# Performance work log

Hardware: AMD Instinct MI355X
Metric: run time of the kernel (lower is better)

The kernel has to match this reference:

```python
import jax, jax.numpy as jnp
import numpy as np

N_NODES = 50000
BN_EPS = 1e-5


def setup_inputs() -> dict:
    key = jax.random.key(0)
    ks = jax.random.split(key, 16)
    N, IN, H, OUT, E = N_NODES, 512, 128, 64, 800000
    s = lambda fi, fo: 1.0 / np.sqrt(fi)
    inp = {
        'x': jax.random.normal(ks[0], (N, IN), dtype=jnp.float32),
        'edge_index': jax.random.randint(ks[1], (2, E), 0, N, dtype=jnp.int32),
        # mlpA: Linear(N -> H)
        'WA': jax.random.uniform(ks[2], (H, N), jnp.float32, -s(N, H), s(N, H)),
        'bA': jax.random.uniform(ks[3], (H,), jnp.float32, -s(N, H), s(N, H)),
        # mlpX: Linear(IN -> H)
        'WX': jax.random.uniform(ks[4], (H, IN), jnp.float32, -s(IN, H), s(IN, H)),
        'bX': jax.random.uniform(ks[5], (H,), jnp.float32, -s(IN, H), s(IN, H)),
        # W: Linear(2H -> H)
        'W': jax.random.uniform(ks[6], (H, 2 * H), jnp.float32, -s(2 * H, H), s(2 * H, H)),
        'bW': jax.random.uniform(ks[7], (H,), jnp.float32, -s(2 * H, H), s(2 * H, H)),
        # mlp_final layer 1: Linear(H -> H) + BN
        'Wf1': jax.random.uniform(ks[8], (H, H), jnp.float32, -s(H, H), s(H, H)),
        'bf1': jax.random.uniform(ks[9], (H,), jnp.float32, -s(H, H), s(H, H)),
        'gamma': jnp.ones((H,), jnp.float32),
        'beta': jnp.zeros((H,), jnp.float32),
        # mlp_final layer 2: Linear(H -> OUT)
        'Wf2': jax.random.uniform(ks[10], (OUT, H), jnp.float32, -s(H, OUT), s(H, OUT)),
        'bf2': jax.random.uniform(ks[11], (OUT,), jnp.float32, -s(H, OUT), s(H, OUT)),
    }
    return inp


def _batchnorm(x, gamma, beta):
    # training-mode BN over the node/batch axis (biased variance, as in torch)
    mean = jnp.mean(x, axis=0)
    var = jnp.var(x, axis=0)
    return (x - mean) * jax.lax.rsqrt(var + BN_EPS) * gamma + beta


def reference(x, edge_index, WA, bA, WX, bX, W, bW, Wf1, bf1, gamma, beta, Wf2, bf2):
    row, col = edge_index[0], edge_index[1]
    row = row - row.min()
    # xA = A @ WA.T + bA  where A[i,j]=1 per (row,col) edge (duplicates sum).
    # Equivalent SpMM: gather columns of WA at `col`, segment-sum into `row`.
    xA = jax.ops.segment_sum(WA.T[col], row, num_segments=N_NODES) + bA  # [N, H]
    xX = x @ WX.T + bX  # [N, H]
    h = jnp.concatenate([xA, xX], axis=-1) @ W.T + bW  # [N, H]
    h = jax.nn.relu(h + xA + xX)
    # mlp_final (num_layers=2): Linear -> ReLU -> BN -> (dropout off) -> Linear
    h = jax.nn.relu(h @ Wf1.T + bf1)
    h = _batchnorm(h, gamma, beta)
    out = h @ Wf2.T + bf2  # [N, OUT]
    return out
```

## Files before the change

### kernel.cpp

```cpp
#include <hip/hip_runtime.h>

typedef __bf16 bf16_t;
typedef __bf16 bf16x8 __attribute__((ext_vector_type(8)));
typedef float f32x4 __attribute__((ext_vector_type(4)));

#define IN_DIM 512
#define H_DIM 128
#define OUT_DIM 64
#define BN_EPS 1e-5f
#define SCAN_BLK 2048

__device__ __forceinline__ float ld_adapt(const void* p, size_t i, int isbf) {
    return isbf ? (float)((const bf16_t*)p)[i] : ((const float*)p)[i];
}

__device__ __forceinline__ void split8(const float* __restrict__ p, bf16x8& hi, bf16x8& lo) {
    f32x4 v0 = *(const f32x4*)p;
    f32x4 v1 = *(const f32x4*)(p + 4);
#pragma unroll
    for (int i = 0; i < 8; ++i) {
        float f = (i < 4) ? v0[i] : v1[i - 4];
        bf16_t h = (bf16_t)f;
        hi[i] = h;
        lo[i] = (bf16_t)(f - (float)h);
    }
}

__global__ void k_init(const void* bA, const void* bX, const void* bW, const void* bf1,
                       const void* gamma, const void* beta, const void* bf2,
                       float* __restrict__ dst, int* __restrict__ flag) {
    __shared__ int s_isbf;
    if (threadIdx.x == 0) {
        unsigned u = *(const unsigned*)gamma;
        int f = (u == 0x3F803F80u) ? 1 : 0;
        *flag = f;
        s_isbf = f;
    }
    __syncthreads();
    int isbf = s_isbf;
    int t = threadIdx.x;
    dst[t] = ld_adapt(bA, t, isbf);
    dst[128 + t] = ld_adapt(bX, t, isbf);
    dst[256 + t] = ld_adapt(bW, t, isbf);
    dst[384 + t] = ld_adapt(bf1, t, isbf);
    dst[512 + t] = ld_adapt(gamma, t, isbf);
    dst[640 + t] = ld_adapt(beta, t, isbf);
    if (t < OUT_DIM) dst[768 + t] = ld_adapt(bf2, t, isbf);
}

__global__ __launch_bounds__(256) void k_transpose(const void* __restrict__ WA,
                                                   float* __restrict__ WAT, int N,
                                                   const int* __restrict__ flag) {
    __shared__ float t[64][130];
    int isbf = *flag;
    int n0 = blockIdx.x * 64;
    int tid = threadIdx.x;
#pragma unroll
    for (int i = 0; i < 32; ++i) {
        int lin = i * 256 + tid;
        int h = lin >> 6, nl = lin & 63;
        int n = n0 + nl;
        t[nl][h] = (n < N) ? ld_adapt(WA, (size_t)h * N + n, isbf) : 0.f;
    }
    __syncthreads();
#pragma unroll
    for (int i = 0; i < 32; ++i) {
        int lin = i * 256 + tid;
        int nl = lin >> 7, h = lin & 127;
        int n = n0 + nl;
        if (n < N) WAT[(size_t)n * H_DIM + h] = t[nl][h];
    }
}

__global__ __launch_bounds__(256) void k_prep(const int* __restrict__ rows, int E,
                                              int* __restrict__ bmin, int* __restrict__ cnt) {
    __shared__ int sm[4];
    int i = blockIdx.x * 256 + threadIdx.x;
    int m = 0x7fffffff;
    if (i < E) {
        int r = rows[i];
        m = r;
        atomicAdd(&cnt[r], 1);
    }
    for (int off = 32; off; off >>= 1) m = min(m, __shfl_xor(m, off, 64));
    if ((threadIdx.x & 63) == 0) sm[threadIdx.x >> 6] = m;
    __syncthreads();
    if (threadIdx.x == 0)
        bmin[blockIdx.x] = min(min(sm[0], sm[1]), min(sm[2], sm[3]));
}

__global__ __launch_bounds__(256) void k_scan1(const int* __restrict__ cnt,
                                               int* __restrict__ offs,
                                               int* __restrict__ bsum, int N) {
    __shared__ int ts[256];
    int base = blockIdx.x * SCAN_BLK;
    int t = threadIdx.x;
    int v[8], s = 0;
#pragma unroll
    for (int i = 0; i < 8; ++i) {
        int idx = base + t * 8 + i;
        v[i] = (idx < N) ? cnt[idx] : 0;
        s += v[i];
    }
    ts[t] = s;
    __syncthreads();
    for (int off = 1; off < 256; off <<= 1) {
        int x = (t >= off) ? ts[t - off] : 0;
        __syncthreads();
        ts[t] += x;
        __syncthreads();
    }
    int run = ts[t] - s;
#pragma unroll
    for (int i = 0; i < 8; ++i) {
        int idx = base + t * 8 + i;
        if (idx < N) offs[idx] = run;
        run += v[i];
    }
    if (t == 255) bsum[blockIdx.x] = ts[255];
}

__global__ __launch_bounds__(256) void k_scan2(int* __restrict__ bsum, int* __restrict__ offs,
                                               int NB, int N, const int* __restrict__ bmin,
                                               int nbmin, int* __restrict__ minbuf) {
    __shared__ int sm[256];
    int t = threadIdx.x;
    int m = 0x7fffffff;
    for (int i = t; i < nbmin; i += 256) m = min(m, bmin[i]);
    sm[t] = m;
    __syncthreads();
    for (int off = 128; off; off >>= 1) {
        if (t < off) sm[t] = min(sm[t], sm[t + off]);
        __syncthreads();
    }
    if (t == 0) {
        *minbuf = sm[0];
        int run = 0;
        for (int b = 0; b < NB; ++b) {
            int v = bsum[b];
            bsum[b] = run;
            run += v;
        }
        offs[N] = run;
    }
}

__global__ __launch_bounds__(256) void k_scan3(int* __restrict__ offs, const int* __restrict__ bsum,
                                               int* __restrict__ cursor, int N) {
    int i = blockIdx.x * 256 + threadIdx.x;
    if (i >= N) return;
    int v = offs[i] + bsum[i / SCAN_BLK];
    offs[i] = v;
    cursor[i] = v;
}

__global__ __launch_bounds__(256) void k_build(const int* __restrict__ rows,
                                               const int* __restrict__ cols, int E,
                                               int* __restrict__ cursor,
                                               int* __restrict__ scol) {
    int i = blockIdx.x * 256 + threadIdx.x;
    if (i >= E) return;
    int r = rows[i];
    int pos = atomicAdd(&cursor[r], 1);
    scol[pos] = cols[i];
}

__global__ __launch_bounds__(256) void k_gather(const int* __restrict__ offs,
                                                const int* __restrict__ scol,
                                                const float* __restrict__ WAT,
                                                const float* __restrict__ bA_f,
                                                const int* __restrict__ minbuf,
                                                float* __restrict__ xA, int N) {
    int wave = threadIdx.x >> 6, lane = threadIdx.x & 63;
    int r = blockIdx.x * 4 + wave;
    if (r >= N) return;
    int b = r + *minbuf;
    int s = 0, e = 0;
    if (b < N) {
        s = offs[b];
        e = offs[b + 1];
    }
    float2 a0 = {0.f, 0.f}, a1 = {0.f, 0.f};
    int i = s;
    for (; i + 3 < e; i += 4) {
        int c0 = scol[i], c1 = scol[i + 1], c2 = scol[i + 2], c3 = scol[i + 3];
        float2 w0 = *(const float2*)(WAT + (size_t)c0 * H_DIM + lane * 2);
        float2 w1 = *(const float2*)(WAT + (size_t)c1 * H_DIM + lane * 2);
        float2 w2 = *(const float2*)(WAT + (size_t)c2 * H_DIM + lane * 2);
        float2 w3 = *(const float2*)(WAT + (size_t)c3 * H_DIM + lane * 2);
        a0.x += w0.x + w2.x; a0.y += w0.y + w2.y;
        a1.x += w1.x + w3.x; a1.y += w1.y + w3.y;
    }
    for (; i < e; ++i) {
        int c = scol[i];
        float2 w = *(const float2*)(WAT + (size_t)c * H_DIM + lane * 2);
        a0.x += w.x; a0.y += w.y;
    }
    float2 bias = *(const float2*)(bA_f + lane * 2);
    float2 out = {a0.x + a1.x + bias.x, a0.y + a1.y + bias.y};
    *(float2*)(xA + (size_t)r * H_DIM + lane * 2) = out;
}

__device__ __forceinline__ void pack_frag(const void* __restrict__ W, bf16_t* __restrict__ hi,
                                          bf16_t* __restrict__ lo, int K, int NC,
                                          const float* __restrict__ scale, int addres, int isbf,
                                          int f, int lane) {
    int ks = f / (NC >> 4), nt = f % (NC >> 4);
    int n = nt * 16 + (lane & 15);
    int k0 = ks * 32 + (lane >> 4) * 8;
    bf16_t* dh = hi + (size_t)f * 512 + lane * 8;
    bf16_t* dl = lo + (size_t)f * 512 + lane * 8;
#pragma unroll
    for (int j = 0; j < 8; ++j) {
        int kk = k0 + j;
        float v = ld_adapt(W, (size_t)n * K + kk, isbf);
        if (scale) v *= scale[kk];
        if (addres && (kk == n || kk == n + H_DIM)) v += 1.f;
        bf16_t h = (bf16_t)v;
        dh[j] = h;
        dl[j] = (bf16_t)(v - (float)h);
    }
}

__global__ __launch_bounds__(256) void k_pack3(const void* WX, bf16_t* WXh, bf16_t* WXl,
                                               const void* W, bf16_t* Wh, bf16_t* Wl,
                                               const void* Wf1, bf16_t* Wf1h, bf16_t* Wf1l,
                                               const int* __restrict__ flag) {
    int g = blockIdx.x * 256 + threadIdx.x;
    int f = g >> 6, lane = g & 63;
    int isbf = *flag;
    if (f < 128)
        pack_frag(WX, WXh, WXl, IN_DIM, H_DIM, nullptr, 0, isbf, f, lane);
    else if (f < 192)
        pack_frag(W, Wh, Wl, 2 * H_DIM, H_DIM, nullptr, 1, isbf, f - 128, lane);
    else if (f < 224)
        pack_frag(Wf1, Wf1h, Wf1l, H_DIM, H_DIM, nullptr, 0, isbf, f - 192, lane);
}

__global__ __launch_bounds__(256) void k_pack(const void* __restrict__ W, bf16_t* __restrict__ hi,
                                              bf16_t* __restrict__ lo, int K, int NC,
                                              const float* __restrict__ scale,
                                              const int* __restrict__ flag) {
    int g = blockIdx.x * 256 + threadIdx.x;
    int f = g >> 6, lane = g & 63;
    int nfrag = (K >> 5) * (NC >> 4);
    if (f >= nfrag) return;
    pack_frag(W, hi, lo, K, NC, scale, 0, *flag, f, lane);
}

template <int KS_TOT, int KS_A, int NT, int MODE, bool ADAPT>
__global__ __launch_bounds__(256) void k_gemm(
    const void* __restrict__ A1v, const float* __restrict__ A2, int astride,
    const bf16_t* __restrict__ Bh, const bf16_t* __restrict__ Bl,
    const float* __restrict__ bias, void* __restrict__ dstv, int dstride,
    double* __restrict__ sums, double* __restrict__ sumsq,
    const int* __restrict__ flag, int M) {
    int tid = threadIdx.x;
    int wave = tid >> 6, lane = tid & 63;
    int l16 = lane & 15, quad = lane >> 4;
    int mbase = blockIdx.x * 128 + wave * 32;
    int isbf = *flag;

    f32x4 acc[2][NT] = {};
    int r0 = min(mbase + l16, M - 1);
    int r1 = min(mbase + 16 + l16, M - 1);
    size_t off0 = (size_t)r0 * astride + quad * 8;
    size_t off1 = (size_t)r1 * astride + quad * 8;

    bf16x8 zero8;
#pragma unroll
    for (int i = 0; i < 8; ++i) zero8[i] = (bf16_t)0.f;

    for (int ks = 0; ks < KS_TOT; ++ks) {
        bf16x8 ah0, al0, ah1, al1;
        if (ADAPT && isbf) {
            const bf16_t* bp = (const bf16_t*)A1v;
            ah0 = *(const bf16x8*)(bp + off0 + ks * 32);
            ah1 = *(const bf16x8*)(bp + off1 + ks * 32);
            al0 = zero8;
            al1 = zero8;
        } else {
            const float* fp;
            int kk;
            if (ks < KS_A) { fp = (const float*)A1v; kk = ks; }
            else { fp = A2; kk = ks - KS_A; }
            split8(fp + off0 + kk * 32, ah0, al0);
            split8(fp + off1 + kk * 32, ah1, al1);
        }
        const bf16_t* bhp = Bh + (size_t)ks * NT * 512 + lane * 8;
        const bf16_t* blp = Bl + (size_t)ks * NT * 512 + lane * 8;
#pragma unroll
        for (int nt = 0; nt < NT; ++nt) {
            bf16x8 bh = *(const bf16x8*)(bhp + (size_t)nt * 512);
            bf16x8 bl = *(const bf16x8*)(blp + (size_t)nt * 512);
            acc[0][nt] = __builtin_amdgcn_mfma_f32_16x16x32_bf16(ah0, bh, acc[0][nt], 0, 0, 0);
            acc[1][nt] = __builtin_amdgcn_mfma_f32_16x16x32_bf16(ah1, bh, acc[1][nt], 0, 0, 0);
            acc[0][nt] = __builtin_amdgcn_mfma_f32_16x16x32_bf16(ah0, bl, acc[0][nt], 0, 0, 0);
            acc[1][nt] = __builtin_amdgcn_mfma_f32_16x16x32_bf16(ah1, bl, acc[1][nt], 0, 0, 0);
            acc[0][nt] = __builtin_amdgcn_mfma_f32_16x16x32_bf16(al0, bh, acc[0][nt], 0, 0, 0);
            acc[1][nt] = __builtin_amdgcn_mfma_f32_16x16x32_bf16(al1, bh, acc[1][nt], 0, 0, 0);
        }
    }

    float* dst = (float*)dstv;
#pragma unroll
    for (int nt = 0; nt < NT; ++nt) {
        int col = nt * 16 + l16;
        float s = 0.f, s2 = 0.f;
#pragma unroll
        for (int ms = 0; ms < 2; ++ms) {
#pragma unroll
            for (int r = 0; r < 4; ++r) {
                int row = mbase + ms * 16 + quad * 4 + r;
                if (row >= M) continue;
                float v = acc[ms][nt][r] + bias[col];
                if (MODE == 1) {
                    v = fmaxf(v, 0.f);
                } else if (MODE == 2) {
                    v = fmaxf(v, 0.f);
                    s += v;
                    s2 += v * v;
                }
                if (MODE == 3) {
                    if (isbf)
                        ((bf16_t*)dstv)[(size_t)row * dstride + col] = (bf16_t)v;
                    else
                        dst[(size_t)row * dstride + col] = v;
                } else {
                    dst[(size_t)row * dstride + col] = v;
                }
            }
        }
        if (MODE == 2) {
            s += __shfl_xor(s, 16, 64);
            s += __shfl_xor(s, 32, 64);
            s2 += __shfl_xor(s2, 16, 64);
            s2 += __shfl_xor(s2, 32, 64);
            if (quad == 0) {
                atomicAdd(&sums[col], (double)s);
                atomicAdd(&sumsq[col], (double)s2);
            }
        }
    }
}

__global__ void k_stats(const double* __restrict__ sums, const double* __restrict__ sumsq,
                        const float* __restrict__ gamma_f, const float* __restrict__ beta_f,
                        const void* __restrict__ Wf2, const float* __restrict__ bf2_f,
                        float* __restrict__ aw, float* __restrict__ bf2w,
                        const int* __restrict__ flag, int N) {
    __shared__ float cs[H_DIM];
    int t = threadIdx.x;
    int isbf = *flag;
    if (t < H_DIM) {
        double mean = sums[t] / (double)N;
        double var = sumsq[t] / (double)N - mean * mean;
        if (var < 0) var = 0;
        float a = gamma_f[t] * rsqrtf((float)var + BN_EPS);
        aw[t] = a;
        cs[t] = beta_f[t] - (float)mean * a;
    }
    __syncthreads();
    if (t < OUT_DIM) {
        float acc = bf2_f[t];
        for (int j = 0; j < H_DIM; ++j) acc += ld_adapt(Wf2, (size_t)t * H_DIM + j, isbf) * cs[j];
        bf2w[t] = acc;
    }
}

extern "C" void kernel_launch(void* const* d_in, const int* in_sizes, int n_in,
                              void* d_out, int out_size, void* d_ws, size_t ws_size,
                              hipStream_t stream) {
    const void* x = d_in[0];
    const int* ei = (const int*)d_in[1];
    const void* WA = d_in[2];
    const void* bA = d_in[3];
    const void* WX = d_in[4];
    const void* bX = d_in[5];
    const void* W = d_in[6];
    const void* bW = d_in[7];
    const void* Wf1 = d_in[8];
    const void* bf1 = d_in[9];
    const void* gamma = d_in[10];
    const void* beta = d_in[11];
    const void* Wf2 = d_in[12];
    const void* bf2 = d_in[13];

    const int N = in_sizes[0] / IN_DIM;
    const int E = in_sizes[1] / 2;
    const int* rows = ei;
    const int* cols = ei + E;
    const int eblocks = (E + 255) / 256;

    char* ws = (char*)d_ws;
    size_t off = 0;
    auto alloc = [&](size_t bytes) {
        char* p = ws + off;
        off += (bytes + 255) & ~(size_t)255;
        return p;
    };
    int* flag = (int*)alloc(4);
    int* minbuf = (int*)alloc(4);
    float* smallf = (float*)alloc(832 * 4);
    double* sums = (double*)alloc(2 * H_DIM * 8);
    double* sumsq = sums + H_DIM;
    float* aw = (float*)alloc(H_DIM * 4);
    float* bf2w = (float*)alloc(OUT_DIM * 4);
    bf16_t* WXp_h = (bf16_t*)alloc((size_t)IN_DIM * H_DIM * 2);
    bf16_t* WXp_l = (bf16_t*)alloc((size_t)IN_DIM * H_DIM * 2);
    bf16_t* Wp_h = (bf16_t*)alloc((size_t)256 * H_DIM * 2);
    bf16_t* Wp_l = (bf16_t*)alloc((size_t)256 * H_DIM * 2);
    bf16_t* Wf1p_h = (bf16_t*)alloc((size_t)H_DIM * H_DIM * 2);
    bf16_t* Wf1p_l = (bf16_t*)alloc((size_t)H_DIM * H_DIM * 2);
    bf16_t* Wf2p_h = (bf16_t*)alloc((size_t)H_DIM * OUT_DIM * 2);
    bf16_t* Wf2p_l = (bf16_t*)alloc((size_t)H_DIM * OUT_DIM * 2);
    int* cnt = (int*)alloc((size_t)N * 4);
    int* offs = (int*)alloc(((size_t)N + 1) * 4);
    int* cursor = (int*)alloc((size_t)N * 4);
    int* bsum = (int*)alloc(64 * 4);
    int* bmin = (int*)alloc((size_t)eblocks * 4);
    int* scol = (int*)alloc((size_t)E * 4);
    float* WAT = (float*)alloc((size_t)N * H_DIM * 4);
    float* xAf = (float*)alloc((size_t)N * H_DIM * 4);
    float* xXf = (float*)alloc((size_t)N * H_DIM * 4);
    float* h1 = WAT;
    float* h2 = xAf;

    float* bA_f = smallf + 0;
    float* bX_f = smallf + 128;
    float* bW_f = smallf + 256;
    float* bf1_f = smallf + 384;
    float* gamma_f = smallf + 512;
    float* beta_f = smallf + 640;
    float* bf2_f = smallf + 768;

    hipMemsetAsync(cnt, 0, (size_t)N * 4, stream);
    hipMemsetAsync(sums, 0, 2 * H_DIM * 8, stream);

    k_init<<<1, 128, 0, stream>>>(bA, bX, bW, bf1, gamma, beta, bf2, smallf, flag);
    k_transpose<<<(N + 63) / 64, 256, 0, stream>>>(WA, WAT, N, flag);
    k_pack3<<<56, 256, 0, stream>>>(WX, WXp_h, WXp_l, W, Wp_h, Wp_l, Wf1, Wf1p_h, Wf1p_l, flag);

    k_prep<<<eblocks, 256, 0, stream>>>(rows, E, bmin, cnt);
    int NB = (N + SCAN_BLK - 1) / SCAN_BLK;
    k_scan1<<<NB, 256, 0, stream>>>(cnt, offs, bsum, N);
    k_scan2<<<1, 256, 0, stream>>>(bsum, offs, NB, N, bmin, eblocks, minbuf);
    k_scan3<<<(N + 255) / 256, 256, 0, stream>>>(offs, bsum, cursor, N);
    k_build<<<eblocks, 256, 0, stream>>>(rows, cols, E, cursor, scol);
    k_gather<<<(N + 3) / 4, 256, 0, stream>>>(offs, scol, WAT, bA_f, minbuf, xAf, N);

    int gblocks = (N + 127) / 128;
    k_gemm<16, 16, 8, 0, true><<<gblocks, 256, 0, stream>>>(
        x, nullptr, IN_DIM, WXp_h, WXp_l, bX_f, xXf, H_DIM, nullptr, nullptr, flag, N);
    k_gemm<8, 4, 8, 1, false><<<gblocks, 256, 0, stream>>>(
        xAf, xXf, H_DIM, Wp_h, Wp_l, bW_f, h1, H_DIM, nullptr, nullptr, flag, N);
    k_gemm<4, 4, 8, 2, false><<<gblocks, 256, 0, stream>>>(
        h1, nullptr, H_DIM, Wf1p_h, Wf1p_l, bf1_f, h2, H_DIM, sums, sumsq, flag, N);
    k_stats<<<1, 128, 0, stream>>>(sums, sumsq, gamma_f, beta_f, Wf2, bf2_f, aw, bf2w, flag, N);
    k_pack<<<4, 256, 0, stream>>>(Wf2, Wf2p_h, Wf2p_l, H_DIM, OUT_DIM, aw, flag);
    k_gemm<4, 4, 4, 3, false><<<gblocks, 256, 0, stream>>>(
        h2, nullptr, H_DIM, Wf2p_h, Wf2p_l, bf2w, d_out, OUT_DIM, nullptr, nullptr, flag, N);
}
```

Baseline: 526.6 us.

## Fuse three dense GEMMs into one kernel and fold BN stats/pack into final GEMM

Merges the x@WX, concat@W and Wf1 GEMMs into a single kernel that keeps the intermediate 16-row tiles in shared memory instead of writing xX and h1 to global memory. BN statistics are first reduced per block in shared memory before the double atomics. The stats, Wf2 packing and final GEMM become one kernel that recomputes the scale and packs Wf2 into LDS in every block. This removes several launches and large intermediate round trips, but it halves rows per wave (16 instead of 32), so there is less reuse of B fragments, and every block redundantly repacks Wf2.

```diff
diff --git a/kernel.cpp b/kernel.cpp
--- a/kernel.cpp
+++ b/kernel.cpp
@@ -10,11 +10,13 @@
 #define BN_EPS 1e-5f
 #define SCAN_BLK 2048
 
+#define MFMA(a, b, c) __builtin_amdgcn_mfma_f32_16x16x32_bf16(a, b, c, 0, 0, 0)
+
 __device__ __forceinline__ float ld_adapt(const void* p, size_t i, int isbf) {
     return isbf ? (float)((const bf16_t*)p)[i] : ((const float*)p)[i];
 }
 
-__device__ __forceinline__ void split8(const float* __restrict__ p, bf16x8& hi, bf16x8& lo) {
+__device__ __forceinline__ void split8(const float* p, bf16x8& hi, bf16x8& lo) {
     f32x4 v0 = *(const f32x4*)p;
     f32x4 v1 = *(const f32x4*)(p + 4);
 #pragma unroll
@@ -203,8 +205,7 @@
 
 __device__ __forceinline__ void pack_frag(const void* __restrict__ W, bf16_t* __restrict__ hi,
                                           bf16_t* __restrict__ lo, int K, int NC,
-                                          const float* __restrict__ scale, int addres, int isbf,
-                                          int f, int lane) {
+                                          int addres, int isbf, int f, int lane) {
     int ks = f / (NC >> 4), nt = f % (NC >> 4);
     int n = nt * 16 + (lane & 15);
     int k0 = ks * 32 + (lane >> 4) * 8;
@@ -214,7 +215,6 @@
     for (int j = 0; j < 8; ++j) {
         int kk = k0 + j;
         float v = ld_adapt(W, (size_t)n * K + kk, isbf);
-        if (scale) v *= scale[kk];
         if (addres && (kk == n || kk == n + H_DIM)) v += 1.f;
         bf16_t h = (bf16_t)v;
         dh[j] = h;
@@ -230,141 +230,232 @@
     int f = g >> 6, lane = g & 63;
     int isbf = *flag;
     if (f < 128)
-        pack_frag(WX, WXh, WXl, IN_DIM, H_DIM, nullptr, 0, isbf, f, lane);
+        pack_frag(WX, WXh, WXl, IN_DIM, H_DIM, 0, isbf, f, lane);
     else if (f < 192)
-        pack_frag(W, Wh, Wl, 2 * H_DIM, H_DIM, nullptr, 1, isbf, f - 128, lane);
+        pack_frag(W, Wh, Wl, 2 * H_DIM, H_DIM, 1, isbf, f - 128, lane);
     else if (f < 224)
-        pack_frag(Wf1, Wf1h, Wf1l, H_DIM, H_DIM, nullptr, 0, isbf, f - 192, lane);
-}
-
-__global__ __launch_bounds__(256) void k_pack(const void* __restrict__ W, bf16_t* __restrict__ hi,
-                                              bf16_t* __restrict__ lo, int K, int NC,
-                                              const float* __restrict__ scale,
-                                              const int* __restrict__ flag) {
-    int g = blockIdx.x * 256 + threadIdx.x;
-    int f = g >> 6, lane = g & 63;
-    int nfrag = (K >> 5) * (NC >> 4);
-    if (f >= nfrag) return;
-    pack_frag(W, hi, lo, K, NC, scale, 0, *flag, f, lane);
-}
-
-template <int KS_TOT, int KS_A, int NT, int MODE, bool ADAPT>
-__global__ __launch_bounds__(256) void k_gemm(
-    const void* __restrict__ A1v, const float* __restrict__ A2, int astride,
-    const bf16_t* __restrict__ Bh, const bf16_t* __restrict__ Bl,
-    const float* __restrict__ bias, void* __restrict__ dstv, int dstride,
+        pack_frag(Wf1, Wf1h, Wf1l, H_DIM, H_DIM, 0, isbf, f - 192, lane);
+}
+
+__global__ __launch_bounds__(256) void k_fuseA(
+    const void* __restrict__ x, const float* __restrict__ xAf,
+    const bf16_t* __restrict__ WXh, const bf16_t* __restrict__ WXl,
+    const bf16_t* __restrict__ Wh, const bf16_t* __restrict__ Wl,
+    const bf16_t* __restrict__ Wf1h, const bf16_t* __restrict__ Wf1l,
+    const float* __restrict__ smallf, float* __restrict__ h2,
     double* __restrict__ sums, double* __restrict__ sumsq,
     const int* __restrict__ flag, int M) {
+    __shared__ float axx[4][16 * 132];
+    __shared__ float ls_sum[H_DIM], ls_sq[H_DIM];
     int tid = threadIdx.x;
-    int wave = tid >> 6, lane = tid & 63;
-    int l16 = lane & 15, quad = lane >> 4;
-    int mbase = blockIdx.x * 128 + wave * 32;
+    int wave = tid >> 6, lane = tid & 63, l16 = lane & 15, quad = lane >> 4;
+    int mbase = blockIdx.x * 64 + wave * 16;
     int isbf = *flag;
-
-    f32x4 acc[2][NT] = {};
+    float* ax = axx[wave];
     int r0 = min(mbase + l16, M - 1);
-    int r1 = min(mbase + 16 + l16, M - 1);
-    size_t off0 = (size_t)r0 * astride + quad * 8;
-    size_t off1 = (size_t)r1 * astride + quad * 8;
+    const float* bX = smallf + 128;
+    const float* bW = smallf + 256;
+    const float* bf1 = smallf + 384;
+
+    if (tid < H_DIM) {
+        ls_sum[tid] = 0.f;
+        ls_sq[tid] = 0.f;
+    }
+    __syncthreads();
 
     bf16x8 zero8;
 #pragma unroll
     for (int i = 0; i < 8; ++i) zero8[i] = (bf16_t)0.f;
 
-    for (int ks = 0; ks < KS_TOT; ++ks) {
-        bf16x8 ah0, al0, ah1, al1;
-        if (ADAPT && isbf) {
-            const bf16_t* bp = (const bf16_t*)A1v;
-            ah0 = *(const bf16x8*)(bp + off0 + ks * 32);
-            ah1 = *(const bf16x8*)(bp + off1 + ks * 32);
-            al0 = zero8;
-            al1 = zero8;
-        } else {
-            const float* fp;
-            int kk;
-            if (ks < KS_A) { fp = (const float*)A1v; kk = ks; }
-            else { fp = A2; kk = ks - KS_A; }
-            split8(fp + off0 + kk * 32, ah0, al0);
-            split8(fp + off1 + kk * 32, ah1, al1);
-        }
-        const bf16_t* bhp = Bh + (size_t)ks * NT * 512 + lane * 8;
-        const bf16_t* blp = Bl + (size_t)ks * NT * 512 + lane * 8;
-#pragma unroll
-        for (int nt = 0; nt < NT; ++nt) {
-            bf16x8 bh = *(const bf16x8*)(bhp + (size_t)nt * 512);
-            bf16x8 bl = *(const bf16x8*)(blp + (size_t)nt * 512);
-            acc[0][nt] = __builtin_amdgcn_mfma_f32_16x16x32_bf16(ah0, bh, acc[0][nt], 0, 0, 0);
-            acc[1][nt] = __builtin_amdgcn_mfma_f32_16x16x32_bf16(ah1, bh, acc[1][nt], 0, 0, 0);
-            acc[0][nt] = __builtin_amdgcn_mfma_f32_16x16x32_bf16(ah0, bl, acc[0][nt], 0, 0, 0);
-            acc[1][nt] = __builtin_amdgcn_mfma_f32_16x16x32_bf16(ah1, bl, acc[1][nt], 0, 0, 0);
-            acc[0][nt] = __builtin_amdgcn_mfma_f32_16x16x32_bf16(al0, bh, acc[0][nt], 0, 0, 0);
-            acc[1][nt] = __builtin_amdgcn_mfma_f32_16x16x32_bf16(al1, bh, acc[1][nt], 0, 0, 0);
-        }
-    }
-
-    float* dst = (float*)dstv;
-#pragma unroll
-    for (int nt = 0; nt < NT; ++nt) {
+    f32x4 acc[8];
+#pragma unroll
+    for (int nt = 0; nt < 8; ++nt) acc[nt] = f32x4{0.f, 0.f, 0.f, 0.f};
+    {
+        size_t offx = (size_t)r0 * IN_DIM + quad * 8;
+        for (int ks = 0; ks < 16; ++ks) {
+            bf16x8 ah, al;
+            if (isbf) {
+                ah = *(const bf16x8*)((const bf16_t*)x + offx + ks * 32);
+                al = zero8;
+            } else {
+                split8((const float*)x + offx + ks * 32, ah, al);
+            }
+            const bf16_t* bhp = WXh + (size_t)ks * 8 * 512 + lane * 8;
+            const bf16_t* blp = WXl + (size_t)ks * 8 * 512 + lane * 8;
+#pragma unroll
+            for (int nt = 0; nt < 8; ++nt) {
+                bf16x8 bh = *(const bf16x8*)(bhp + nt * 512);
+                bf16x8 bl = *(const bf16x8*)(blp + nt * 512);
+                acc[nt] = MFMA(ah, bh, acc[nt]);
+                acc[nt] = MFMA(ah, bl, acc[nt]);
+                acc[nt] = MFMA(al, bh, acc[nt]);
+            }
+        }
+    }
+#pragma unroll
+    for (int nt = 0; nt < 8; ++nt) {
         int col = nt * 16 + l16;
+        float b = bX[col];
+#pragma unroll
+        for (int r = 0; r < 4; ++r) {
+            int lr = quad * 4 + r;
+            ax[lr * 132 + col] = acc[nt][r] + b;
+        }
+    }
+
+#pragma unroll
+    for (int nt = 0; nt < 8; ++nt) acc[nt] = f32x4{0.f, 0.f, 0.f, 0.f};
+    for (int ks = 0; ks < 8; ++ks) {
+        bf16x8 ah, al;
+        if (ks < 4)
+            split8(xAf + (size_t)r0 * H_DIM + ks * 32 + quad * 8, ah, al);
+        else
+            split8(ax + l16 * 132 + (ks - 4) * 32 + quad * 8, ah, al);
+        const bf16_t* bhp = Wh + (size_t)ks * 8 * 512 + lane * 8;
+        const bf16_t* blp = Wl + (size_t)ks * 8 * 512 + lane * 8;
+#pragma unroll
+        for (int nt = 0; nt < 8; ++nt) {
+            bf16x8 bh = *(const bf16x8*)(bhp + nt * 512);
+            bf16x8 bl = *(const bf16x8*)(blp + nt * 512);
+            acc[nt] = MFMA(ah, bh, acc[nt]);
+            acc[nt] = MFMA(ah, bl, acc[nt]);
+            acc[nt] = MFMA(al, bh, acc[nt]);
+        }
+    }
+#pragma unroll
+    for (int nt = 0; nt < 8; ++nt) {
+        int col = nt * 16 + l16;
+        float b = bW[col];
+#pragma unroll
+        for (int r = 0; r < 4; ++r) {
+            int lr = quad * 4 + r;
+            ax[lr * 132 + col] = fmaxf(acc[nt][r] + b, 0.f);
+        }
+    }
+
+#pragma unroll
+    for (int nt = 0; nt < 8; ++nt) acc[nt] = f32x4{0.f, 0.f, 0.f, 0.f};
+    for (int ks = 0; ks < 4; ++ks) {
+        bf16x8 ah, al;
+        split8(ax + l16 * 132 + ks * 32 + quad * 8, ah, al);
+        const bf16_t* bhp = Wf1h + (size_t)ks * 8 * 512 + lane * 8;
+        const bf16_t* blp = Wf1l + (size_t)ks * 8 * 512 + lane * 8;
+#pragma unroll
+        for (int nt = 0; nt < 8; ++nt) {
+            bf16x8 bh = *(const bf16x8*)(bhp + nt * 512);
+            bf16x8 bl = *(const bf16x8*)(blp + nt * 512);
+            acc[nt] = MFMA(ah, bh, acc[nt]);
+            acc[nt] = MFMA(ah, bl, acc[nt]);
+            acc[nt] = MFMA(al, bh, acc[nt]);
+        }
+    }
+#pragma unroll
+    for (int nt = 0; nt < 8; ++nt) {
+        int col = nt * 16 + l16;
+        float b = bf1[col];
         float s = 0.f, s2 = 0.f;
 #pragma unroll
-        for (int ms = 0; ms < 2; ++ms) {
-#pragma unroll
-            for (int r = 0; r < 4; ++r) {
-                int row = mbase + ms * 16 + quad * 4 + r;
-                if (row >= M) continue;
-                float v = acc[ms][nt][r] + bias[col];
-                if (MODE == 1) {
-                    v = fmaxf(v, 0.f);
-                } else if (MODE == 2) {
-                    v = fmaxf(v, 0.f);
-                    s += v;
-                    s2 += v * v;
-                }
-                if (MODE == 3) {
-                    if (isbf)
-                        ((bf16_t*)dstv)[(size_t)row * dstride + col] = (bf16_t)v;
-                    else
-                        dst[(size_t)row * dstride + col] = v;
-                } else {
-                    dst[(size_t)row * dstride + col] = v;
-                }
+        for (int r = 0; r < 4; ++r) {
+            int row = mbase + quad * 4 + r;
+            if (row < M) {
+                float v = fmaxf(acc[nt][r] + b, 0.f);
+                h2[(size_t)row * H_DIM + col] = v;
+                s += v;
+                s2 += v * v;
             }
         }
-        if (MODE == 2) {
-            s += __shfl_xor(s, 16, 64);
-            s += __shfl_xor(s, 32, 64);
-            s2 += __shfl_xor(s2, 16, 64);
-            s2 += __shfl_xor(s2, 32, 64);
-            if (quad == 0) {
-                atomicAdd(&sums[col], (double)s);
-                atomicAdd(&sumsq[col], (double)s2);
-            }
-        }
-    }
-}
-
-__global__ void k_stats(const double* __restrict__ sums, const double* __restrict__ sumsq,
-                        const float* __restrict__ gamma_f, const float* __restrict__ beta_f,
-                        const void* __restrict__ Wf2, const float* __restrict__ bf2_f,
-                        float* __restrict__ aw, float* __restrict__ bf2w,
-                        const int* __restrict__ flag, int N) {
-    __shared__ float cs[H_DIM];
+        s += __shfl_xor(s, 16, 64);
+        s += __shfl_xor(s, 32, 64);
+        s2 += __shfl_xor(s2, 16, 64);
+        s2 += __shfl_xor(s2, 32, 64);
+        if (quad == 0) {
+            atomicAdd(&ls_sum[col], s);
+            atomicAdd(&ls_sq[col], s2);
+        }
+    }
+    __syncthreads();
+    if (tid < H_DIM) {
+        atomicAdd(&sums[tid], (double)ls_sum[tid]);
+        atomicAdd(&sumsq[tid], (double)ls_sq[tid]);
+    }
+}
+
+__global__ __launch_bounds__(256) void k_fuseB(
+    const float* __restrict__ h2, const void* __restrict__ Wf2,
+    const float* __restrict__ smallf, const double* __restrict__ sums,
+    const double* __restrict__ sumsq, void* __restrict__ outv,
+    const int* __restrict__ flag, int M) {
+    __shared__ bf16_t wh[16 * 512];
+    __shared__ bf16_t wl[16 * 512];
+    __shared__ float aw[H_DIM], cw[H_DIM], b2[OUT_DIM];
     int t = threadIdx.x;
     int isbf = *flag;
+    const float* gamma_f = smallf + 512;
+    const float* beta_f = smallf + 640;
+    const float* bf2_f = smallf + 768;
+
     if (t < H_DIM) {
-        double mean = sums[t] / (double)N;
-        double var = sumsq[t] / (double)N - mean * mean;
+        double mean = sums[t] / (double)M;
+        double var = sumsq[t] / (double)M - mean * mean;
         if (var < 0) var = 0;
         float a = gamma_f[t] * rsqrtf((float)var + BN_EPS);
         aw[t] = a;
-        cs[t] = beta_f[t] - (float)mean * a;
+        cw[t] = beta_f[t] - (float)mean * a;
     }
     __syncthreads();
     if (t < OUT_DIM) {
         float acc = bf2_f[t];
-        for (int j = 0; j < H_DIM; ++j) acc += ld_adapt(Wf2, (size_t)t * H_DIM + j, isbf) * cs[j];
-        bf2w[t] = acc;
+        for (int j = 0; j < H_DIM; ++j) acc += ld_adapt(Wf2, (size_t)t * H_DIM + j, isbf) * cw[j];
+        b2[t] = acc;
+    }
+    for (int u = t; u < 1024; u += 256) {
+        int f = u >> 6, ln = u & 63;
+        int ks = f >> 2, nt = f & 3;
+        int n = nt * 16 + (ln & 15);
+        int k0 = ks * 32 + (ln >> 4) * 8;
+#pragma unroll
+        for (int j = 0; j < 8; ++j) {
+            float v = ld_adapt(Wf2, (size_t)n * H_DIM + k0 + j, isbf) * aw[k0 + j];
+            bf16_t h = (bf16_t)v;
+            wh[f * 512 + ln * 8 + j] = h;
+            wl[f * 512 + ln * 8 + j] = (bf16_t)(v - (float)h);
+        }
+    }
+    __syncthreads();
+
+    int wave = t >> 6, lane = t & 63, l16 = lane & 15, quad = lane >> 4;
+    int mbase = blockIdx.x * 64 + wave * 16;
+    int r0 = min(mbase + l16, M - 1);
+    f32x4 acc4[4];
+#pragma unroll
+    for (int nt = 0; nt < 4; ++nt) acc4[nt] = f32x4{0.f, 0.f, 0.f, 0.f};
+    for (int ks = 0; ks < 4; ++ks) {
+        bf16x8 ah, al;
+        split8(h2 + (size_t)r0 * H_DIM + ks * 32 + quad * 8, ah, al);
+#pragma unroll
+        for (int nt = 0; nt < 4; ++nt) {
+            bf16x8 bh = *(const bf16x8*)(wh + (ks * 4 + nt) * 512 + lane * 8);
+            bf16x8 bl = *(const bf16x8*)(wl + (ks * 4 + nt) * 512 + lane * 8);
+            acc4[nt] = MFMA(ah, bh, acc4[nt]);
+            acc4[nt] = MFMA(ah, bl, acc4[nt]);
+            acc4[nt] = MFMA(al, bh, acc4[nt]);
+        }
+    }
+#pragma unroll
+    for (int nt = 0; nt < 4; ++nt) {
+        int col = nt * 16 + l16;
+        float b = b2[col];
+#pragma unroll
+        for (int r = 0; r < 4; ++r) {
+            int row = mbase + quad * 4 + r;
+            if (row < M) {
+                float v = acc4[nt][r] + b;
+                if (isbf)
+                    ((bf16_t*)outv)[(size_t)row * OUT_DIM + col] = (bf16_t)v;
+                else
+                    ((float*)outv)[(size_t)row * OUT_DIM + col] = v;
+            }
+        }
     }
 }
 
@@ -404,16 +495,12 @@
     float* smallf = (float*)alloc(832 * 4);
     double* sums = (double*)alloc(2 * H_DIM * 8);
     double* sumsq = sums + H_DIM;
-    float* aw = (float*)alloc(H_DIM * 4);
-    float* bf2w = (float*)alloc(OUT_DIM * 4);
     bf16_t* WXp_h = (bf16_t*)alloc((size_t)IN_DIM * H_DIM * 2);
     bf16_t* WXp_l = (bf16_t*)alloc((size_t)IN_DIM * H_DIM * 2);
     bf16_t* Wp_h = (bf16_t*)alloc((size_t)256 * H_DIM * 2);
     bf16_t* Wp_l = (bf16_t*)alloc((size_t)256 * H_DIM * 2);
     bf16_t* Wf1p_h = (bf16_t*)alloc((size_t)H_DIM * H_DIM * 2);
     bf16_t* Wf1p_l = (bf16_t*)alloc((size_t)H_DIM * H_DIM * 2);
-    bf16_t* Wf2p_h = (bf16_t*)alloc((size_t)H_DIM * OUT_DIM * 2);
-    bf16_t* Wf2p_l = (bf16_t*)alloc((size_t)H_DIM * OUT_DIM * 2);
     int* cnt = (int*)alloc((size_t)N * 4);
     int* offs = (int*)alloc(((size_t)N + 1) * 4);
     int* cursor = (int*)alloc((size_t)N * 4);
@@ -422,17 +509,9 @@
     int* scol = (int*)alloc((size_t)E * 4);
     float* WAT = (float*)alloc((size_t)N * H_DIM * 4);
     float* xAf = (float*)alloc((size_t)N * H_DIM * 4);
-    float* xXf = (float*)alloc((size_t)N * H_DIM * 4);
-    float* h1 = WAT;
-    float* h2 = xAf;
+    float* h2 = WAT;
 
     float* bA_f = smallf + 0;
-    float* bX_f = smallf + 128;
-    float* bW_f = smallf + 256;
-    float* bf1_f = smallf + 384;
-    float* gamma_f = smallf + 512;
-    float* beta_f = smallf + 640;
-    float* bf2_f = smallf + 768;
 
     hipMemsetAsync(cnt, 0, (size_t)N * 4, stream);
     hipMemsetAsync(sums, 0, 2 * H_DIM * 8, stream);
@@ -449,15 +528,8 @@
     k_build<<<eblocks, 256, 0, stream>>>(rows, cols, E, cursor, scol);
     k_gather<<<(N + 3) / 4, 256, 0, stream>>>(offs, scol, WAT, bA_f, minbuf, xAf, N);
 
-    int gblocks = (N + 127) / 128;
-    k_gemm<16, 16, 8, 0, true><<<gblocks, 256, 0, stream>>>(
-        x, nullptr, IN_DIM, WXp_h, WXp_l, bX_f, xXf, H_DIM, nullptr, nullptr, flag, N);
-    k_gemm<8, 4, 8, 1, false><<<gblocks, 256, 0, stream>>>(
-        xAf, xXf, H_DIM, Wp_h, Wp_l, bW_f, h1, H_DIM, nullptr, nullptr, flag, N);
-    k_gemm<4, 4, 8, 2, false><<<gblocks, 256, 0, stream>>>(
-        h1, nullptr, H_DIM, Wf1p_h, Wf1p_l, bf1_f, h2, H_DIM, sums, sumsq, flag, N);
-    k_stats<<<1, 128, 0, stream>>>(sums, sumsq, gamma_f, beta_f, Wf2, bf2_f, aw, bf2w, flag, N);
-    k_pack<<<4, 256, 0, stream>>>(Wf2, Wf2p_h, Wf2p_l, H_DIM, OUT_DIM, aw, flag);
-    k_gemm<4, 4, 4, 3, false><<<gblocks, 256, 0, stream>>>(
-        h2, nullptr, H_DIM, Wf2p_h, Wf2p_l, bf2w, d_out, OUT_DIM, nullptr, nullptr, flag, N);
-}
+    int fblocks = (N + 63) / 64;
+    k_fuseA<<<fblocks, 256, 0, stream>>>(x, xAf, WXp_h, WXp_l, Wp_h, Wp_l, Wf1p_h, Wf1p_l,
+                                         smallf, h2, sums, sumsq, flag, N);
+    k_fuseB<<<fblocks, 256, 0, stream>>>(h2, Wf2, smallf, sums, sumsq, d_out, flag, N);
+}
```

Result: faster. 484.8 us (-7.9%).
